# Kernel tuning notes

Hardware: AMD Instinct MI355X
Metric: run time of the kernel (lower is better)

The kernel has to match this reference:

```python
import jax, jax.numpy as jnp
import numpy as np

LN_EPS = 1e-5
BN_EPS = 1e-5


def setup_inputs() -> dict:
    key = jax.random.key(0)
    ks = jax.random.split(key, 16)
    b, n = 16, 256
    sc = 0.1
    inp = {
        "x": jax.random.normal(ks[0], (b, n, 4), jnp.float32),
        # proj: Linear(4, 64)
        "proj_w": jax.random.normal(ks[1], (4, 64), jnp.float32) * sc,
        "proj_b": jnp.zeros((64,), jnp.float32),
        # sigma_net: Linear(128,64) -> LayerNorm(64) -> ReLU -> Linear(64,1) -> Softplus
        "s_w1": jax.random.normal(ks[2], (128, 64), jnp.float32) * sc,
        "s_b1": jnp.zeros((64,), jnp.float32),
        "ln_g": jnp.ones((64,), jnp.float32),
        "ln_b": jnp.zeros((64,), jnp.float32),
        "s_w2": jax.random.normal(ks[3], (64, 1), jnp.float32) * sc,
        "s_b2": jnp.zeros((1,), jnp.float32),
        # gnn weight
        "gnn_w": jax.random.normal(ks[4], (64, 64), jnp.float32) * sc,
        # classifier: Linear(128,64) -> BatchNorm1d(64) -> ELU -> Dropout(eval) -> Linear(64,2)
        "c_w1": jax.random.normal(ks[5], (128, 64), jnp.float32) * sc,
        "c_b1": jnp.zeros((64,), jnp.float32),
        "bn_g": jnp.ones((64,), jnp.float32),
        "bn_b": jnp.zeros((64,), jnp.float32),
        "bn_mean": jnp.zeros((64,), jnp.float32),
        "bn_var": jnp.ones((64,), jnp.float32),
        "c_w2": jax.random.normal(ks[6], (64, 2), jnp.float32) * sc,
        "c_b2": jnp.zeros((2,), jnp.float32),
    }
    return inp


def reference(x, proj_w, proj_b, s_w1, s_b1, ln_g, ln_b, s_w2, s_b2,
              gnn_w, c_w1, c_b1, bn_g, bn_b, bn_mean, bn_var, c_w2, c_b2):
    # h: [b, n, 64]
    h = jax.nn.elu(x @ proj_w + proj_b)

    # sigma_net(cat([xi, xj])) == hi @ s_w1[:64] + hj @ s_w1[64:] + s_b1, broadcast pairwise
    a_i = h @ s_w1[:64]            # [b, n, 64]
    a_j = h @ s_w1[64:]            # [b, n, 64]
    pre = a_i[:, :, None, :] + a_j[:, None, :, :] + s_b1  # [b, n, n, 64]
    mu = jnp.mean(pre, axis=-1, keepdims=True)
    var = jnp.mean((pre - mu) ** 2, axis=-1, keepdims=True)
    ln = (pre - mu) * jax.lax.rsqrt(var + LN_EPS) * ln_g + ln_b
    sig_pre = jax.nn.relu(ln) @ s_w2 + s_b2               # [b, n, n, 1]
    sigmas = jax.nn.softplus(sig_pre[..., 0])             # [b, n, n]

    # squared pairwise distance via gram trick: ||hi - hj||^2
    sq = jnp.sum(h * h, axis=-1)                          # [b, n]
    gram = jnp.einsum("bid,bjd->bij", h, h)               # [b, n, n]
    d2 = jnp.maximum(sq[:, :, None] + sq[:, None, :] - 2.0 * gram, 0.0)
    adj = jnp.exp(-d2 / (2.0 * sigmas ** 2 + 1e-6))       # [b, n, n]

    h_agg = jnp.einsum("bij,bjd->bid", adj, h) @ gnn_w    # [b, n, 64]
    h_res = jax.nn.elu(h_agg + h)

    pooled = jnp.concatenate([h_res.mean(axis=1), h_res.max(axis=1)], axis=1)  # [b, 128]

    z = pooled @ c_w1 + c_b1
    z = (z - bn_mean) * jax.lax.rsqrt(bn_var + BN_EPS) * bn_g + bn_b  # BN eval mode
    z = jax.nn.elu(z)                                      # Dropout is identity in eval
    return z @ c_w2 + c_b2                                 # [b, 2]
```

## Files before the change

kernel.cpp:

```cpp
#include <hip/hip_runtime.h>
#include <math.h>


#define OFF_H      0
#define OFF_HT     262144
#define OFF_AI     (262144*2)
#define OFF_AJT    (262144*3)
#define OFF_SQ     (262144*4)
#define OFF_HAGG   (262144*4 + 4096)
#define OFF_HRES   (262144*5 + 4096)

__device__ __forceinline__ float elu_f(float x) { return x > 0.f ? x : expm1f(x); }

__global__ __launch_bounds__(256) void k1_embed(
    const float* __restrict__ x,
    const float* __restrict__ proj_w, const float* __restrict__ proj_b,
    const float* __restrict__ s_w1, const float* __restrict__ s_b1,
    float* __restrict__ h, float* __restrict__ hT,
    float* __restrict__ a_i, float* __restrict__ a_jT,
    float* __restrict__ sq)
{
    int lane = threadIdx.x & 63;
    int wave = threadIdx.x >> 6;
    int row  = blockIdx.x * 4 + wave;
    int b = row >> 8, i = row & 255;

    __shared__ float hsh[4][64];

    float x0 = x[row*4+0], x1 = x[row*4+1], x2 = x[row*4+2], x3 = x[row*4+3];
    float hv = x0*proj_w[lane] + x1*proj_w[64+lane] + x2*proj_w[128+lane]
             + x3*proj_w[192+lane] + proj_b[lane];
    hv = elu_f(hv);
    hsh[wave][lane] = hv;
    __syncthreads();

    float ai = s_b1[lane], aj = 0.f, sqv = 0.f;
    #pragma unroll
    for (int e = 0; e < 64; ++e) {
        float he = hsh[wave][e];
        ai  += he * s_w1[e*64 + lane];
        aj  += he * s_w1[(64+e)*64 + lane];
        sqv += he * he;
    }
    h[row*64 + lane] = hv;
    hT[b*64*256 + lane*256 + i] = hv;
    a_i[row*64 + lane] = ai;
    a_jT[b*64*256 + lane*256 + i] = aj;
    if (lane == 0) sq[row] = sqv;
}

#define TI 4
__global__ __launch_bounds__(256) void k2_pair(
    const float* __restrict__ a_i, const float* __restrict__ a_jT,
    const float* __restrict__ hT, const float* __restrict__ h,
    const float* __restrict__ sq,
    const float* __restrict__ ln_g, const float* __restrict__ ln_b,
    const float* __restrict__ s_w2, const float* __restrict__ s_b2,
    float* __restrict__ h_agg)
{
    int bi0 = blockIdx.x * TI;
    int b   = bi0 >> 8;
    int j   = threadIdx.x;

    __shared__ float ai_sh[TI][64], hi_sh[TI][64];
    __shared__ float g_sh[64], be_sh[64], w2_sh[64];
    __shared__ float adj_sh[256][TI];
    __shared__ float part_sh[4][TI][64];

    if (j < 64) { g_sh[j] = ln_g[j]; be_sh[j] = ln_b[j]; w2_sh[j] = s_w2[j]; }
    {
        int i = j >> 6, d = j & 63;
        ai_sh[i][d] = a_i[(bi0 + i)*64 + d];
        hi_sh[i][d] = h[(bi0 + i)*64 + d];
    }
    __syncthreads();

    const float* ajb = a_jT + b*64*256;
    const float* htb = hT   + b*64*256;

    float ps[TI], pss[TI], dt[TI];
    #pragma unroll
    for (int i = 0; i < TI; ++i) { ps[i] = 0.f; pss[i] = 0.f; dt[i] = 0.f; }
    #pragma unroll 8
    for (int d = 0; d < 64; ++d) {
        float ajd = ajb[d*256 + j];
        float hjd = htb[d*256 + j];
        #pragma unroll
        for (int i = 0; i < TI; ++i) {
            float pre = ai_sh[i][d] + ajd;
            ps[i]  += pre;
            pss[i]  = fmaf(pre, pre, pss[i]);
            dt[i]   = fmaf(hi_sh[i][d], hjd, dt[i]);
        }
    }
    float rs[TI], nmurs[TI];
    #pragma unroll
    for (int i = 0; i < TI; ++i) {
        float mu  = ps[i] * (1.f/64.f);
        float var = pss[i] * (1.f/64.f) - mu*mu;
        rs[i]    = rsqrtf(var + 1e-5f);
        nmurs[i] = -mu * rs[i];
    }

    float acc[TI];
    #pragma unroll
    for (int i = 0; i < TI; ++i) acc[i] = 0.f;
    #pragma unroll 8
    for (int d = 0; d < 64; ++d) {
        float ajd = ajb[d*256 + j];
        float gd = g_sh[d], bd = be_sh[d], wd = w2_sh[d];
        #pragma unroll
        for (int i = 0; i < TI; ++i) {
            float pre = ai_sh[i][d] + ajd;
            float v   = fmaf(pre, rs[i], nmurs[i]);
            float t   = fmaf(v, gd, bd);
            t = fmaxf(t, 0.f);
            acc[i] = fmaf(t, wd, acc[i]);
        }
    }

    float b2  = s_b2[0];
    float sqj = sq[b*256 + j];
    #pragma unroll
    for (int i = 0; i < TI; ++i) {
        float sp  = acc[i] + b2;
        float sig = fmaxf(sp, 0.f) + log1pf(expf(-fabsf(sp)));
        float sqi = sq[bi0 + i];
        float d2  = fmaxf(sqi + sqj - 2.f*dt[i], 0.f);
        adj_sh[j][i] = expf(-d2 / (2.f*sig*sig + 1e-6f));
    }
    __syncthreads();

    int d = j & 63, q = j >> 6;
    const float* hb = h + b*256*64;
    float part[TI];
    #pragma unroll
    for (int i = 0; i < TI; ++i) part[i] = 0.f;
    #pragma unroll 8
    for (int k = 0; k < 64; ++k) {
        int jj = q*64 + k;
        float hv = hb[jj*64 + d];
        float4 a4 = *(const float4*)&adj_sh[jj][0];
        part[0] = fmaf(a4.x, hv, part[0]);
        part[1] = fmaf(a4.y, hv, part[1]);
        part[2] = fmaf(a4.z, hv, part[2]);
        part[3] = fmaf(a4.w, hv, part[3]);
    }
    #pragma unroll
    for (int i = 0; i < TI; ++i) part_sh[q][i][d] = part[i];
    __syncthreads();
    {
        int i = j >> 6, dd = j & 63;
        float v = part_sh[0][i][dd] + part_sh[1][i][dd]
                + part_sh[2][i][dd] + part_sh[3][i][dd];
        h_agg[(bi0 + i)*64 + dd] = v;
    }
}

__global__ __launch_bounds__(256) void k3_gnn(
    const float* __restrict__ h_agg, const float* __restrict__ h,
    const float* __restrict__ gnn_w, float* __restrict__ h_res)
{
    int lane = threadIdx.x & 63, wave = threadIdx.x >> 6;
    int row = blockIdx.x*4 + wave;
    __shared__ float agg_sh[4][64];
    agg_sh[wave][lane] = h_agg[row*64 + lane];
    __syncthreads();
    float acc = 0.f;
    #pragma unroll
    for (int e = 0; e < 64; ++e)
        acc += agg_sh[wave][e] * gnn_w[e*64 + lane];
    float v = elu_f(acc + h[row*64 + lane]);
    h_res[row*64 + lane] = v;
}

__global__ __launch_bounds__(256) void k4_pool_cls(
    const float* __restrict__ h_res,
    const float* __restrict__ c_w1, const float* __restrict__ c_b1,
    const float* __restrict__ bn_g, const float* __restrict__ bn_b,
    const float* __restrict__ bn_mean, const float* __restrict__ bn_var,
    const float* __restrict__ c_w2, const float* __restrict__ c_b2,
    float* __restrict__ out)
{
    int b = blockIdx.x;
    int tid = threadIdx.x;
    int d = tid & 63, q = tid >> 6;
    const float* hb = h_res + b*256*64;

    float sum = 0.f, mx = -INFINITY;
    #pragma unroll 8
    for (int k = 0; k < 64; ++k) {
        float v = hb[(q*64+k)*64 + d];
        sum += v; mx = fmaxf(mx, v);
    }
    __shared__ float sum_sh[256], max_sh[256];
    __shared__ float pm_sh[64], px_sh[64];
    sum_sh[tid] = sum; max_sh[tid] = mx;
    __syncthreads();
    if (tid < 64) {
        float tsum = sum_sh[tid] + sum_sh[64+tid] + sum_sh[128+tid] + sum_sh[192+tid];
        float tmax = fmaxf(fmaxf(max_sh[tid], max_sh[64+tid]),
                           fmaxf(max_sh[128+tid], max_sh[192+tid]));
        pm_sh[tid] = tsum * (1.f/256.f);
        px_sh[tid] = tmax;
    }
    __syncthreads();
    if (tid < 64) {
        float acc = c_b1[tid];
        #pragma unroll
        for (int e = 0; e < 64; ++e) {
            acc += pm_sh[e] * c_w1[e*64 + tid];
            acc += px_sh[e] * c_w1[(64+e)*64 + tid];
        }
        float z = (acc - bn_mean[tid]) * rsqrtf(bn_var[tid] + 1e-5f) * bn_g[tid] + bn_b[tid];
        z = elu_f(z);
        float c0 = z * c_w2[tid*2 + 0];
        float c1 = z * c_w2[tid*2 + 1];
        for (int off = 32; off > 0; off >>= 1) {
            c0 += __shfl_down(c0, off);
            c1 += __shfl_down(c1, off);
        }
        if (tid == 0) {
            out[b*2 + 0] = c0 + c_b2[0];
            out[b*2 + 1] = c1 + c_b2[1];
        }
    }
}

extern "C" void kernel_launch(void* const* d_in, const int* in_sizes, int n_in,
                              void* d_out, int out_size, void* d_ws, size_t ws_size,
                              hipStream_t stream) {
    const float* x       = (const float*)d_in[0];
    const float* proj_w  = (const float*)d_in[1];
    const float* proj_b  = (const float*)d_in[2];
    const float* s_w1    = (const float*)d_in[3];
    const float* s_b1    = (const float*)d_in[4];
    const float* ln_g    = (const float*)d_in[5];
    const float* ln_b    = (const float*)d_in[6];
    const float* s_w2    = (const float*)d_in[7];
    const float* s_b2    = (const float*)d_in[8];
    const float* gnn_w   = (const float*)d_in[9];
    const float* c_w1    = (const float*)d_in[10];
    const float* c_b1    = (const float*)d_in[11];
    const float* bn_g    = (const float*)d_in[12];
    const float* bn_b    = (const float*)d_in[13];
    const float* bn_mean = (const float*)d_in[14];
    const float* bn_var  = (const float*)d_in[15];
    const float* c_w2    = (const float*)d_in[16];
    const float* c_b2    = (const float*)d_in[17];

    float* w = (float*)d_ws;
    float* h     = w + OFF_H;
    float* hT    = w + OFF_HT;
    float* a_i   = w + OFF_AI;
    float* a_jT  = w + OFF_AJT;
    float* sq    = w + OFF_SQ;
    float* h_agg = w + OFF_HAGG;
    float* h_res = w + OFF_HRES;
    float* out   = (float*)d_out;

    k1_embed<<<1024, 256, 0, stream>>>(x, proj_w, proj_b, s_w1, s_b1,
                                       h, hT, a_i, a_jT, sq);
    k2_pair<<<1024, 256, 0, stream>>>(a_i, a_jT, hT, h, sq,
                                      ln_g, ln_b, s_w2, s_b2, h_agg);
    k3_gnn<<<1024, 256, 0, stream>>>(h_agg, h, gnn_w, h_res);
    k4_pool_cls<<<16, 256, 0, stream>>>(h_res, c_w1, c_b1, bn_g, bn_b,
                                        bn_mean, bn_var, c_w2, c_b2, out);
}
```

Baseline: 52.46 us.

## Fuse GNN weight matmul into pair kernel, double row tile, stage s_w1 in LDS

Removes the separate k3_gnn launch by applying gnn_w, the residual add and ELU at the end of k2_pair, so the h_agg round trip through global memory goes away. The pair kernel now handles 8 query rows per block instead of 4, which halves the grid and reuses each a_j/hT load across more rows. k1_embed stages s_w1 in shared memory, processes two rows per wave and broadcasts h with shuffles instead of an LDS buffer. In exchange, each k2 block uses more LDS and registers (16KB for gnn_w plus larger tiles), and both kernels launch only 512 blocks, which may reduce occupancy.

```diff
diff --git a/kernel.cpp b/kernel.cpp
--- a/kernel.cpp
+++ b/kernel.cpp
@@ -1,14 +1,12 @@
 #include <hip/hip_runtime.h>
 #include <math.h>
-
 
 #define OFF_H      0
 #define OFF_HT     262144
 #define OFF_AI     (262144*2)
 #define OFF_AJT    (262144*3)
 #define OFF_SQ     (262144*4)
-#define OFF_HAGG   (262144*4 + 4096)
-#define OFF_HRES   (262144*5 + 4096)
+#define OFF_HRES   (262144*4 + 4096)
 
 __device__ __forceinline__ float elu_f(float x) { return x > 0.f ? x : expm1f(x); }
 
@@ -20,43 +18,55 @@
     float* __restrict__ a_i, float* __restrict__ a_jT,
     float* __restrict__ sq)
 {
-    int lane = threadIdx.x & 63;
-    int wave = threadIdx.x >> 6;
-    int row  = blockIdx.x * 4 + wave;
-    int b = row >> 8, i = row & 255;
-
-    __shared__ float hsh[4][64];
-
-    float x0 = x[row*4+0], x1 = x[row*4+1], x2 = x[row*4+2], x3 = x[row*4+3];
-    float hv = x0*proj_w[lane] + x1*proj_w[64+lane] + x2*proj_w[128+lane]
-             + x3*proj_w[192+lane] + proj_b[lane];
-    hv = elu_f(hv);
-    hsh[wave][lane] = hv;
-    __syncthreads();
-
-    float ai = s_b1[lane], aj = 0.f, sqv = 0.f;
-    #pragma unroll
-    for (int e = 0; e < 64; ++e) {
-        float he = hsh[wave][e];
-        ai  += he * s_w1[e*64 + lane];
-        aj  += he * s_w1[(64+e)*64 + lane];
-        sqv += he * he;
-    }
-    h[row*64 + lane] = hv;
-    hT[b*64*256 + lane*256 + i] = hv;
-    a_i[row*64 + lane] = ai;
-    a_jT[b*64*256 + lane*256 + i] = aj;
-    if (lane == 0) sq[row] = sqv;
-}
-
-#define TI 4
+    __shared__ float w_sh[8192];
+    int tid = threadIdx.x;
+    #pragma unroll
+    for (int r = 0; r < 8; ++r) {
+        float4 v = *(const float4*)&s_w1[(r*256 + tid)*4];
+        *(float4*)&w_sh[(r*256 + tid)*4] = v;
+    }
+    __syncthreads();
+
+    int lane = tid & 63;
+    int wave = tid >> 6;
+    int row0 = blockIdx.x * 8;
+
+    float pw0 = proj_w[lane], pw1 = proj_w[64+lane], pw2 = proj_w[128+lane],
+          pw3 = proj_w[192+lane], pb = proj_b[lane], b1 = s_b1[lane];
+
+    #pragma unroll
+    for (int r = 0; r < 2; ++r) {
+        int row = row0 + wave*2 + r;
+        int b = row >> 8, i = row & 255;
+        float hv = x[row*4+0]*pw0 + x[row*4+1]*pw1 + x[row*4+2]*pw2
+                 + x[row*4+3]*pw3 + pb;
+        hv = elu_f(hv);
+
+        float ai = b1, aj = 0.f, sqv = 0.f;
+        #pragma unroll 8
+        for (int e = 0; e < 64; ++e) {
+            float he = __shfl(hv, e);
+            ai  = fmaf(he, w_sh[e*64 + lane], ai);
+            aj  = fmaf(he, w_sh[(64+e)*64 + lane], aj);
+            sqv = fmaf(he, he, sqv);
+        }
+        h[row*64 + lane] = hv;
+        hT[b*64*256 + lane*256 + i] = hv;
+        a_i[row*64 + lane] = ai;
+        a_jT[b*64*256 + lane*256 + i] = aj;
+        if (lane == 0) sq[row] = sqv;
+    }
+}
+
+#define TI 8
 __global__ __launch_bounds__(256) void k2_pair(
     const float* __restrict__ a_i, const float* __restrict__ a_jT,
     const float* __restrict__ hT, const float* __restrict__ h,
     const float* __restrict__ sq,
     const float* __restrict__ ln_g, const float* __restrict__ ln_b,
     const float* __restrict__ s_w2, const float* __restrict__ s_b2,
-    float* __restrict__ h_agg)
+    const float* __restrict__ gnn_w,
+    float* __restrict__ h_res)
 {
     int bi0 = blockIdx.x * TI;
     int b   = bi0 >> 8;
@@ -66,12 +76,20 @@
     __shared__ float g_sh[64], be_sh[64], w2_sh[64];
     __shared__ float adj_sh[256][TI];
     __shared__ float part_sh[4][TI][64];
+    __shared__ float hagg_sh[TI][64];
+    __shared__ float gnn_sh[4096];
 
     if (j < 64) { g_sh[j] = ln_g[j]; be_sh[j] = ln_b[j]; w2_sh[j] = s_w2[j]; }
-    {
-        int i = j >> 6, d = j & 63;
+    #pragma unroll
+    for (int r = 0; r < 2; ++r) {
+        int idx = r*256 + j;
+        int i = idx >> 6, d = idx & 63;
         ai_sh[i][d] = a_i[(bi0 + i)*64 + d];
         hi_sh[i][d] = h[(bi0 + i)*64 + d];
+    }
+    #pragma unroll
+    for (int r = 0; r < 4; ++r) {
+        *(float4*)&gnn_sh[(r*256 + j)*4] = *(const float4*)&gnn_w[(r*256 + j)*4];
     }
     __syncthreads();
 
@@ -136,42 +154,46 @@
     float part[TI];
     #pragma unroll
     for (int i = 0; i < TI; ++i) part[i] = 0.f;
-    #pragma unroll 8
+    #pragma unroll 4
     for (int k = 0; k < 64; ++k) {
         int jj = q*64 + k;
         float hv = hb[jj*64 + d];
-        float4 a4 = *(const float4*)&adj_sh[jj][0];
-        part[0] = fmaf(a4.x, hv, part[0]);
-        part[1] = fmaf(a4.y, hv, part[1]);
-        part[2] = fmaf(a4.z, hv, part[2]);
-        part[3] = fmaf(a4.w, hv, part[3]);
+        float4 a0 = *(const float4*)&adj_sh[jj][0];
+        float4 a1 = *(const float4*)&adj_sh[jj][4];
+        part[0] = fmaf(a0.x, hv, part[0]);
+        part[1] = fmaf(a0.y, hv, part[1]);
+        part[2] = fmaf(a0.z, hv, part[2]);
+        part[3] = fmaf(a0.w, hv, part[3]);
+        part[4] = fmaf(a1.x, hv, part[4]);
+        part[5] = fmaf(a1.y, hv, part[5]);
+        part[6] = fmaf(a1.z, hv, part[6]);
+        part[7] = fmaf(a1.w, hv, part[7]);
     }
     #pragma unroll
     for (int i = 0; i < TI; ++i) part_sh[q][i][d] = part[i];
     __syncthreads();
+    #pragma unroll
+    for (int r = 0; r < 2; ++r) {
+        int idx = r*256 + j;
+        int i = idx >> 6, dd = idx & 63;
+        hagg_sh[i][dd] = part_sh[0][i][dd] + part_sh[1][i][dd]
+                       + part_sh[2][i][dd] + part_sh[3][i][dd];
+    }
+    __syncthreads();
+
     {
-        int i = j >> 6, dd = j & 63;
-        float v = part_sh[0][i][dd] + part_sh[1][i][dd]
-                + part_sh[2][i][dd] + part_sh[3][i][dd];
-        h_agg[(bi0 + i)*64 + dd] = v;
-    }
-}
-
-__global__ __launch_bounds__(256) void k3_gnn(
-    const float* __restrict__ h_agg, const float* __restrict__ h,
-    const float* __restrict__ gnn_w, float* __restrict__ h_res)
-{
-    int lane = threadIdx.x & 63, wave = threadIdx.x >> 6;
-    int row = blockIdx.x*4 + wave;
-    __shared__ float agg_sh[4][64];
-    agg_sh[wave][lane] = h_agg[row*64 + lane];
-    __syncthreads();
-    float acc = 0.f;
-    #pragma unroll
-    for (int e = 0; e < 64; ++e)
-        acc += agg_sh[wave][e] * gnn_w[e*64 + lane];
-    float v = elu_f(acc + h[row*64 + lane]);
-    h_res[row*64 + lane] = v;
+        int lane = j & 63, wave = j >> 6;
+        int r0 = wave, r1 = wave + 4;
+        float acc0 = 0.f, acc1 = 0.f;
+        #pragma unroll 8
+        for (int e = 0; e < 64; ++e) {
+            float g = gnn_sh[e*64 + lane];
+            acc0 = fmaf(hagg_sh[r0][e], g, acc0);
+            acc1 = fmaf(hagg_sh[r1][e], g, acc1);
+        }
+        h_res[(bi0 + r0)*64 + lane] = elu_f(acc0 + hi_sh[r0][lane]);
+        h_res[(bi0 + r1)*64 + lane] = elu_f(acc1 + hi_sh[r1][lane]);
+    }
 }
 
 __global__ __launch_bounds__(256) void k4_pool_cls(
@@ -255,15 +277,13 @@
     float* a_i   = w + OFF_AI;
     float* a_jT  = w + OFF_AJT;
     float* sq    = w + OFF_SQ;
-    float* h_agg = w + OFF_HAGG;
     float* h_res = w + OFF_HRES;
     float* out   = (float*)d_out;
 
-    k1_embed<<<1024, 256, 0, stream>>>(x, proj_w, proj_b, s_w1, s_b1,
-                                       h, hT, a_i, a_jT, sq);
-    k2_pair<<<1024, 256, 0, stream>>>(a_i, a_jT, hT, h, sq,
-                                      ln_g, ln_b, s_w2, s_b2, h_agg);
-    k3_gnn<<<1024, 256, 0, stream>>>(h_agg, h, gnn_w, h_res);
+    k1_embed<<<512, 256, 0, stream>>>(x, proj_w, proj_b, s_w1, s_b1,
+                                      h, hT, a_i, a_jT, sq);
+    k2_pair<<<512, 256, 0, stream>>>(a_i, a_jT, hT, h, sq,
+                                     ln_g, ln_b, s_w2, s_b2, gnn_w, h_res);
     k4_pool_cls<<<16, 256, 0, stream>>>(h_res, c_w1, c_b1, bn_g, bn_b,
                                         bn_mean, bn_var, c_w2, c_b2, out);
 }
```

Measured after the change: 70.29 us. 1.34x slower.
